# Performance work log

Measured on AMD Instinct MI355X. Metric: run time of the kernel, lower is better.

The kernel has to match this reference:

```python
import jax, jax.numpy as jnp
import numpy as np

N = 20000        # total nodes
E = 240000       # directed edges (avg in-degree 12); self-loops appended in reference
G = 50           # graphs in the batch
NPG = N // G     # nodes per graph
TD = 768         # text embedding dim
HC = 64          # hidden_channels
H = 8            # attention heads for conv1..conv3 (conv4 uses 1 head)
FD = 3 * HC * H + HC  # JK cat dim for num_layers=4
NEG = 0.2        # GATv2 leaky_relu negative slope
EPS = 1e-5       # GraphNorm eps


def setup_inputs() -> dict:
    key = jax.random.key(0)
    ks = iter(jax.random.split(key, 64))

    def w(shape, s=0.05):
        return jax.random.normal(next(ks), shape, dtype=jnp.float32) * s

    z = lambda *s: jnp.zeros(s, jnp.float32)
    o = lambda *s: jnp.ones(s, jnp.float32)

    inp = {
        'x': w((N, TD), 1.0),
        'edge_index': jax.random.randint(next(ks), (2, E), 0, N, dtype=jnp.int32),
        'batch': jnp.arange(N, dtype=jnp.int32) // NPG,
        'ptr': jnp.arange(G + 1, dtype=jnp.int32) * NPG,
        'tp_w': w((TD, HC)), 'tp_b': z(HC),
        'lin_w': w((FD, 1), 0.005), 'lin_b': z(1),
    }
    # GATv2Conv params: lin_l (source), lin_r (target), att, output bias
    for name, ind, heads, concat in [('c1', HC, H, True), ('c2', HC * H, H, True),
                                     ('c3', HC * H, H, True), ('c4', HC * H, 1, False)]:
        inp[name + '_wl'] = w((ind, heads * HC)); inp[name + '_bl'] = z(heads * HC)
        inp[name + '_wr'] = w((ind, heads * HC)); inp[name + '_br'] = z(heads * HC)
        inp[name + '_att'] = w((heads, HC))
        inp[name + '_bias'] = z(heads * HC if concat else HC)
    # GraphNorm params: weight, bias, mean_scale
    for name, d in [('n1', HC * H), ('n2', HC * H), ('n3', HC * H), ('n4', HC)]:
        inp[name + '_w'] = o(d); inp[name + '_b'] = z(d); inp[name + '_ms'] = o(d)
    return inp


def _gatv2(x, src, dst, wl, bl, wr, br, att, bias, heads, concat):
    # GATv2: e_ij = att . leaky_relu(W_l x_j + W_r x_i); alpha = softmax over in-neighbors of i
    xl = (x @ wl + bl).reshape(N, heads, HC)
    xr = (x @ wr + br).reshape(N, heads, HC)
    e = jax.nn.leaky_relu(xl[src] + xr[dst], NEG)           # [E', H, C]
    logit = jnp.einsum('ehc,hc->eh', e, att)                # [E', H]
    m = jax.ops.segment_max(logit, dst, num_segments=N)     # stable scatter-softmax
    p = jnp.exp(logit - m[dst])
    alpha = p / jax.ops.segment_sum(p, dst, num_segments=N)[dst]
    out = jax.ops.segment_sum(xl[src] * alpha[..., None], dst, num_segments=N)
    out = out.reshape(N, heads * HC) if concat else out.mean(axis=1)
    return out + bias


def _gnorm(x, batch, w, b, ms):
    # PyG GraphNorm: per-graph mean (scaled by mean_scale), per-graph std
    cnt = jax.ops.segment_sum(jnp.ones((N,), x.dtype), batch, num_segments=G)[:, None]
    mean = jax.ops.segment_sum(x, batch, num_segments=G) / cnt
    cen = x - ms * mean[batch]
    var = jax.ops.segment_sum(cen * cen, batch, num_segments=G) / cnt
    return w * cen / jnp.sqrt(var + EPS)[batch] + b


def reference(x, tp_w, tp_b,
              c1_wl, c1_bl, c1_wr, c1_br, c1_att, c1_bias,
              c2_wl, c2_bl, c2_wr, c2_br, c2_att, c2_bias,
              c3_wl, c3_bl, c3_wr, c3_br, c3_att, c3_bias,
              c4_wl, c4_bl, c4_wr, c4_br, c4_att, c4_bias,
              n1_w, n1_b, n1_ms, n2_w, n2_b, n2_ms,
              n3_w, n3_b, n3_ms, n4_w, n4_b, n4_ms,
              lin_w, lin_b, edge_index, batch, ptr):
    sl = jnp.arange(N, dtype=edge_index.dtype)
    src = jnp.concatenate([edge_index[0], sl])  # add_self_loops=True
    dst = jnp.concatenate([edge_index[1], sl])

    h = x @ tp_w + tp_b                          # text_proj (dropout = identity in eval)
    h = _gatv2(h, src, dst, c1_wl, c1_bl, c1_wr, c1_br, c1_att, c1_bias, H, True)
    h = jax.nn.elu(_gnorm(h, batch, n1_w, n1_b, n1_ms))
    xs = [h]
    h2 = _gatv2(h, src, dst, c2_wl, c2_bl, c2_wr, c2_br, c2_att, c2_bias, H, True)
    h = jax.nn.elu(_gnorm(h2 + h, batch, n2_w, n2_b, n2_ms))
    xs.append(h)
    h3 = _gatv2(h, src, dst, c3_wl, c3_bl, c3_wr, c3_br, c3_att, c3_bias, H, True)
    h = jax.nn.elu(_gnorm(h3 + h, batch, n3_w, n3_b, n3_ms))
    xs.append(h)
    h = _gnorm(_gatv2(h, src, dst, c4_wl, c4_bl, c4_wr, c4_br, c4_att, c4_bias, 1, False),
               batch, n4_w, n4_b, n4_ms)
    xs.append(h)

    xcat = jnp.concatenate(xs, axis=1)           # JumpingKnowledge cat -> [N, FD]
    out = xcat[ptr[:-1]] @ lin_w + lin_b         # summary node per graph -> [G, 1]
    return out.squeeze(-1)                       # num_classes==2 -> squeeze
```

## Files before the change

### kernel.cpp

```cpp
#include <hip/hip_runtime.h>
#include <hip/hip_bf16.h>

#define NEG_SLOPE 0.2f
#define EPSI 1e-5f
#define THR 8.0f

typedef __attribute__((ext_vector_type(8))) short bf16x8;
typedef __attribute__((ext_vector_type(4))) float f32x4;
typedef __attribute__((ext_vector_type(2))) float f32x2;

__device__ __forceinline__ float wred_sum(float v){
#pragma unroll
  for (int o = 32; o > 0; o >>= 1) v += __shfl_xor(v, o);
  return v;
}

__device__ __forceinline__ unsigned short f2bf(float f){
  __hip_bfloat16 h = __float2bfloat16(f);
  return *reinterpret_cast<unsigned short*>(&h);
}
__device__ __forceinline__ float bf2f(unsigned short u){
  return __uint_as_float((unsigned int)u << 16);
}
__device__ __forceinline__ f32x2 bfpair(unsigned int u){
  f32x2 r;
  r.x = __uint_as_float(u << 16);
  r.y = __uint_as_float(u & 0xffff0000u);
  return r;
}
__device__ __forceinline__ f32x2 vmax2(f32x2 a, f32x2 b){
#if __has_builtin(__builtin_elementwise_max)
  return __builtin_elementwise_max(a, b);
#else
  f32x2 r; r.x = fmaxf(a.x, b.x); r.y = fmaxf(a.y, b.y); return r;
#endif
}

__device__ __forceinline__ void gload16(const void* g, void* l){
  __builtin_amdgcn_global_load_lds((const __attribute__((address_space(1))) unsigned int*)g,
                                   (__attribute__((address_space(3))) unsigned int*)l, 16, 0, 0);
}

__global__ __launch_bounds__(256) void k_count(const int* __restrict__ ei, int* __restrict__ deg,
                                               int E, int EP){
  int e = blockIdx.x * 256 + threadIdx.x;
  if (e >= EP) return;
  int d = (e < E) ? ei[E + e] : (e - E);
  atomicAdd(&deg[d], 1);
}

__global__ __launch_bounds__(256) void k_scan(int* __restrict__ deg, int* __restrict__ rowptr, int n){
  __shared__ int part[256];
  int t = threadIdx.x;
  int L = (n + 255) / 256;
  int lo = t * L, hi = min(lo + L, n);
  int s = 0;
  for (int i = lo; i < hi; i++) s += deg[i];
  part[t] = s;
  __syncthreads();
  if (t == 0){
    int acc = 0;
    for (int i = 0; i < 256; i++){ int v = part[i]; part[i] = acc; acc += v; }
  }
  __syncthreads();
  int acc = part[t];
  for (int i = lo; i < hi; i++){
    int d = deg[i];
    rowptr[i] = acc;
    deg[i] = acc;
    acc += d;
  }
  if (t == 255) rowptr[n] = acc;
}

__global__ __launch_bounds__(256) void k_fill(const int* __restrict__ ei, int* __restrict__ cursor,
                                              int* __restrict__ srcn, int E, int EP){
  int e = blockIdx.x * 256 + threadIdx.x;
  if (e >= EP) return;
  int s, d;
  if (e < E){ s = ei[e]; d = ei[E + e]; } else { s = d = e - E; }
  int pos = atomicAdd(&cursor[d], 1);
  srcn[pos] = s;
}

__global__ __launch_bounds__(256) void k_cvt_act(const float* __restrict__ in,
                                                 unsigned short* __restrict__ ob, int total4){
  int i = blockIdx.x * 256 + threadIdx.x;
  if (i >= total4) return;
  float4 v = ((const float4*)in)[i];
  ushort4 o;
  o.x = f2bf(v.x); o.y = f2bf(v.y); o.z = f2bf(v.z); o.w = f2bf(v.w);
  ((ushort4*)ob)[i] = o;
}

__global__ __launch_bounds__(256) void k_cvt_wt(const float* __restrict__ W,
                                                unsigned short* __restrict__ Wt,
                                                int K, int Ncol){
  __shared__ float t[32][33];
  int bx = blockIdx.x, by = blockIdx.y;
  int tx = threadIdx.x & 31, ty = threadIdx.x >> 5;
#pragma unroll
  for (int i = 0; i < 4; i++)
    t[ty + i * 8][tx] = W[(size_t)(by * 32 + ty + i * 8) * Ncol + bx * 32 + tx];
  __syncthreads();
#pragma unroll
  for (int i = 0; i < 4; i++)
    Wt[(size_t)(bx * 32 + ty + i * 8) * K + by * 32 + tx] = f2bf(t[tx][ty + i * 8]);
}

__global__ __launch_bounds__(256) void k_cvt_wt2(const float* __restrict__ Wa,
                                                 const float* __restrict__ Wb,
                                                 unsigned short* __restrict__ Wt,
                                                 int K, int Ncol){
  __shared__ float t[32][33];
  int half = gridDim.x >> 1;
  int isB = blockIdx.x >= half;
  const float* W = isB ? Wb : Wa;
  unsigned short* out = Wt + (isB ? (size_t)Ncol * K : 0);
  int bx = isB ? blockIdx.x - half : blockIdx.x;
  int by = blockIdx.y;
  int tx = threadIdx.x & 31, ty = threadIdx.x >> 5;
#pragma unroll
  for (int i = 0; i < 4; i++)
    t[ty + i * 8][tx] = W[(size_t)(by * 32 + ty + i * 8) * Ncol + bx * 32 + tx];
  __syncthreads();
#pragma unroll
  for (int i = 0; i < 4; i++)
    out[(size_t)(bx * 32 + ty + i * 8) * K + by * 32 + tx] = f2bf(t[tx][ty + i * 8]);
}

template<int BN>
__global__ __launch_bounds__(512) void k_gemm_mfma8(const unsigned short* __restrict__ A,
                                                    const unsigned short* __restrict__ Wt,
                                                    const float* __restrict__ ba,
                                                    const float* __restrict__ bb,
                                                    int bsplit,
                                                    unsigned short* __restrict__ Cb,
                                                    int M, int K, int Ncol){
  constexpr int NF = BN / 64;
  __shared__ unsigned short As[128 * 32];
  __shared__ unsigned short Bs[BN * 32];
  const int tid = threadIdx.x;
  const int w = tid >> 6, lane = tid & 63;
  const int wr = w >> 2, wc = w & 3;
  const int row0 = blockIdx.y * 128, col0 = blockIdx.x * BN;
  const int lr = lane & 15, lk = lane >> 4;
  const int swz = (lr >> 1) & 3;

  f32x4 acc[4][NF];
#pragma unroll
  for (int i = 0; i < 4; i++)
#pragma unroll
    for (int j = 0; j < NF; j++) acc[i][j] = (f32x4){0.f, 0.f, 0.f, 0.f};

  for (int k0 = 0; k0 < K; k0 += 32){
    for (int g0 = w * 64; g0 < 512; g0 += 512){
      int g = g0 + lane;
      int row = g >> 2, slot = g & 3;
      int kq = slot ^ ((row >> 1) & 3);
      int srow = row0 + row; if (srow >= M) srow = M - 1;
      gload16(&A[(size_t)srow * K + k0 + kq * 8], &As[(size_t)g0 * 8]);
    }
    for (int g0 = w * 64; g0 < BN * 4; g0 += 512){
      int g = g0 + lane;
      int col = g >> 2, slot = g & 3;
      int kq = slot ^ ((col >> 1) & 3);
      gload16(&Wt[(size_t)(col0 + col) * K + k0 + kq * 8], &Bs[(size_t)g0 * 8]);
    }
    __syncthreads();

    bf16x8 af[4], bf_[NF];
#pragma unroll
    for (int mi = 0; mi < 4; mi++){
      int rl = wr * 64 + mi * 16 + lr;
      af[mi] = *(const bf16x8*)&As[(rl * 4 + (lk ^ swz)) * 8];
    }
#pragma unroll
    for (int ni = 0; ni < NF; ni++){
      int cl = wc * (BN / 4) + ni * 16 + lr;
      bf_[ni] = *(const bf16x8*)&Bs[(cl * 4 + (lk ^ swz)) * 8];
    }
#pragma unroll
    for (int mi = 0; mi < 4; mi++)
#pragma unroll
      for (int ni = 0; ni < NF; ni++)
        acc[mi][ni] = __builtin_amdgcn_mfma_f32_16x16x32_bf16(af[mi], bf_[ni], acc[mi][ni], 0, 0, 0);
    __syncthreads();
  }

#pragma unroll
  for (int mi = 0; mi < 4; mi++){
#pragma unroll
    for (int ni = 0; ni < NF; ni++){
      int gc = col0 + wc * (BN / 4) + ni * 16 + lr;
      float bv = gc < bsplit ? ba[gc] : bb[gc - bsplit];
#pragma unroll
      for (int r = 0; r < 4; r++){
        int gr = row0 + wr * 64 + mi * 16 + lk * 4 + r;
        if (gr < M) Cb[(size_t)gr * Ncol + gc] = f2bf(acc[mi][ni][r] + bv);
      }
    }
  }
}

__global__ __launch_bounds__(256) void k_gat_fused8(const unsigned short* __restrict__ xlrb,
                                                    const float* __restrict__ att,
                                                    const int* __restrict__ rowptr,
                                                    const int* __restrict__ srcn,
                                                    const float* __restrict__ bias,
                                                    const unsigned short* __restrict__ resb,
                                                    unsigned short* __restrict__ yb,
                                                    int N){
  int node = (blockIdx.x * 256 + threadIdx.x) >> 6;
  int lane = threadIdx.x & 63;
  if (node >= N) return;
  f32x2 xr2[4], av2[4];
  {
    uint4 ur = *(const uint4*)&xlrb[(size_t)node * 1024 + 512 + lane * 8];
    xr2[0] = bfpair(ur.x); xr2[1] = bfpair(ur.y); xr2[2] = bfpair(ur.z); xr2[3] = bfpair(ur.w);
    float4 a0 = *(const float4*)&att[lane * 8];
    float4 a1 = *(const float4*)&att[lane * 8 + 4];
    av2[0] = (f32x2){a0.x, a0.y}; av2[1] = (f32x2){a0.z, a0.w};
    av2[2] = (f32x2){a1.x, a1.y}; av2[3] = (f32x2){a1.z, a1.w};
  }
  int e0 = rowptr[node], e1 = rowptr[node + 1];
  float m0 = -1e30f, s0 = 0.f, m1 = -1e30f, s1 = 0.f;
  f32x2 acc0[4] = {}, acc1[4] = {};

  for (int base = e0; base < e1; base += 64){
    int cnt = min(64, e1 - base);
    int sn = 0;
    if (lane < cnt) sn = srcn[base + lane];
    int k = 0;
    for (; k + 1 < cnt; k += 2){
      int ska = __shfl(sn, k);
      int skb = __shfl(sn, k + 1);
      uint4 ua = *(const uint4*)&xlrb[(size_t)ska * 1024 + lane * 8];
      uint4 ub = *(const uint4*)&xlrb[(size_t)skb * 1024 + lane * 8];
      f32x2 va[4], vb[4];
      va[0] = bfpair(ua.x); va[1] = bfpair(ua.y); va[2] = bfpair(ua.z); va[3] = bfpair(ua.w);
      vb[0] = bfpair(ub.x); vb[1] = bfpair(ub.y); vb[2] = bfpair(ub.z); vb[3] = bfpair(ub.w);
      f32x2 da = (f32x2){0.f, 0.f}, db = (f32x2){0.f, 0.f};
#pragma unroll
      for (int j = 0; j < 4; j++){
        f32x2 ta = va[j] + xr2[j];
        f32x2 tb = vb[j] + xr2[j];
        ta = vmax2(ta, ta * NEG_SLOPE);
        tb = vmax2(tb, tb * NEG_SLOPE);
        da += ta * av2[j];
        db += tb * av2[j];
      }
      float suma = da.x + da.y, sumb = db.x + db.y;
      suma += __shfl_xor(suma, 1); sumb += __shfl_xor(sumb, 1);
      suma += __shfl_xor(suma, 2); sumb += __shfl_xor(sumb, 2);
      suma += __shfl_xor(suma, 4); sumb += __shfl_xor(sumb, 4);
      if (__builtin_expect(__any(suma > m0 + THR), 0)){
        float mn = fmaxf(m0, suma);
        float cs = __expf(m0 - mn);
        float p  = __expf(suma - mn);
        s0 = s0 * cs + p;
#pragma unroll
        for (int j = 0; j < 4; j++) acc0[j] = acc0[j] * cs + va[j] * p;
        m0 = mn;
      } else {
        float p = __expf(suma - m0);
        s0 += p;
#pragma unroll
        for (int j = 0; j < 4; j++) acc0[j] += va[j] * p;
      }
      if (__builtin_expect(__any(sumb > m1 + THR), 0)){
        float mn = fmaxf(m1, sumb);
        float cs = __expf(m1 - mn);
        float p  = __expf(sumb - mn);
        s1 = s1 * cs + p;
#pragma unroll
        for (int j = 0; j < 4; j++) acc1[j] = acc1[j] * cs + vb[j] * p;
        m1 = mn;
      } else {
        float p = __expf(sumb - m1);
        s1 += p;
#pragma unroll
        for (int j = 0; j < 4; j++) acc1[j] += vb[j] * p;
      }
    }
    if (k < cnt){
      int ska = __shfl(sn, k);
      uint4 ua = *(const uint4*)&xlrb[(size_t)ska * 1024 + lane * 8];
      f32x2 va[4];
      va[0] = bfpair(ua.x); va[1] = bfpair(ua.y); va[2] = bfpair(ua.z); va[3] = bfpair(ua.w);
      f32x2 da = (f32x2){0.f, 0.f};
#pragma unroll
      for (int j = 0; j < 4; j++){
        f32x2 ta = va[j] + xr2[j];
        ta = vmax2(ta, ta * NEG_SLOPE);
        da += ta * av2[j];
      }
      float suma = da.x + da.y;
      suma += __shfl_xor(suma, 1);
      suma += __shfl_xor(suma, 2);
      suma += __shfl_xor(suma, 4);
      if (__builtin_expect(__any(suma > m0 + THR), 0)){
        float mn = fmaxf(m0, suma);
        float cs = __expf(m0 - mn);
        float p  = __expf(suma - mn);
        s0 = s0 * cs + p;
#pragma unroll
        for (int j = 0; j < 4; j++) acc0[j] = acc0[j] * cs + va[j] * p;
        m0 = mn;
      } else {
        float p = __expf(suma - m0);
        s0 += p;
#pragma unroll
        for (int j = 0; j < 4; j++) acc0[j] += va[j] * p;
      }
    }
  }
  float m = fmaxf(m0, m1);
  float c0 = __expf(m0 - m), c1 = __expf(m1 - m);
  float s = s0 * c0 + s1 * c1;
  float inv = 1.f / s;
  float4 b0 = *(const float4*)&bias[lane * 8];
  float4 b1 = *(const float4*)&bias[lane * 8 + 4];
  f32x2 bi2[4] = {(f32x2){b0.x, b0.y}, (f32x2){b0.z, b0.w},
                  (f32x2){b1.x, b1.y}, (f32x2){b1.z, b1.w}};
  f32x2 re2[4] = {};
  size_t o = (size_t)node * 512 + lane * 8;
  if (resb){
    uint4 rr = *(const uint4*)&resb[o];
    re2[0] = bfpair(rr.x); re2[1] = bfpair(rr.y); re2[2] = bfpair(rr.z); re2[3] = bfpair(rr.w);
  }
  bf16x8 ov;
#pragma unroll
  for (int j = 0; j < 4; j++){
    f32x2 r = (acc0[j] * c0 + acc1[j] * c1) * inv + bi2[j] + re2[j];
    ov[2 * j]     = (short)f2bf(r.x);
    ov[2 * j + 1] = (short)f2bf(r.y);
  }
  *(bf16x8*)&yb[o] = ov;
}

__global__ __launch_bounds__(256) void k_gat_fused1(const unsigned short* __restrict__ xlr,
                                                    const float* __restrict__ att,
                                                    const int* __restrict__ rowptr,
                                                    const int* __restrict__ srcn,
                                                    const float* __restrict__ bias,
                                                    unsigned short* __restrict__ yb4,
                                                    int N){
  int node = (blockIdx.x * 256 + threadIdx.x) >> 6;
  int lane = threadIdx.x & 63;
  if (node >= N) return;
  float xrv = bf2f(xlr[(size_t)node * 128 + 64 + lane]);
  float attv = att[lane];
  int e0 = rowptr[node], e1 = rowptr[node + 1];
  float m = -1e30f, s = 0.f, acc = 0.f;
  for (int base = e0; base < e1; base += 64){
    int cnt = min(64, e1 - base);
    int sn = 0;
    if (lane < cnt) sn = srcn[base + lane];
    for (int k = 0; k < cnt; k++){
      int sk = __shfl(sn, k);
      float v = bf2f(xlr[(size_t)sk * 128 + lane]);
      float t = v + xrv;
      t = fmaxf(t, t * NEG_SLOPE);
      float sum = wred_sum(t * attv);
      if (sum > m + THR){
        float mn = fmaxf(m, sum);
        float cs = __expf(m - mn);
        float p  = __expf(sum - mn);
        s = s * cs + p;
        acc = acc * cs + p * v;
        m = mn;
      } else {
        float p = __expf(sum - m);
        s += p;
        acc += p * v;
      }
    }
  }
  yb4[(size_t)node * 64 + lane] = f2bf(acc / s + bias[lane]);
}

#define NCHUNK 16
__global__ __launch_bounds__(256) void k_gnorm_stats(const unsigned short* __restrict__ y,
                                                     const int* __restrict__ ptrg,
                                                     float* __restrict__ psum,
                                                     float* __restrict__ psq,
                                                     int OD){
  int g = blockIdx.x, chunk = blockIdx.z;
  int lane = threadIdx.x & 63, sub = threadIdx.x >> 6;
  int c = blockIdx.y * 64 + lane;
  int lo = ptrg[g], hi = ptrg[g + 1], len = hi - lo;
  int c0 = lo + (len * chunk) / NCHUNK, c1 = lo + (len * (chunk + 1)) / NCHUNK;
  float s = 0.f, q = 0.f;
  for (int i = c0 + sub; i < c1; i += 4){
    float v = bf2f(y[(size_t)i * OD + c]);
    s += v; q += v * v;
  }
  __shared__ float sm[4][64], sq2[4][64];
  sm[sub][lane] = s; sq2[sub][lane] = q;
  __syncthreads();
  if (sub == 0){
    s = sm[0][lane] + sm[1][lane] + sm[2][lane] + sm[3][lane];
    q = sq2[0][lane] + sq2[1][lane] + sq2[2][lane] + sq2[3][lane];
    size_t o = (size_t)(g * NCHUNK + chunk) * OD + c;
    psum[o] = s; psq[o] = q;
  }
}

__global__ __launch_bounds__(256) void k_gnorm_coef(const float* __restrict__ psum,
                                                    const float* __restrict__ psq,
                                                    const float* __restrict__ w,
                                                    const float* __restrict__ b,
                                                    const float* __restrict__ ms,
                                                    const int* __restrict__ ptrg,
                                                    float* __restrict__ cA,
                                                    float* __restrict__ cC,
                                                    int OD){
  int g = blockIdx.x;
  int len = ptrg[g + 1] - ptrg[g];
  float inv_n = 1.f / (float)len;
  for (int c = threadIdx.x; c < OD; c += 256){
    float s = 0.f, q = 0.f;
    for (int k = 0; k < NCHUNK; k++){
      size_t o = (size_t)(g * NCHUNK + k) * OD + c;
      s += psum[o]; q += psq[o];
    }
    float mean = s * inv_n, ey2 = q * inv_n;
    float m = ms[c];
    float var = ey2 - mean * mean * (2.f * m - m * m);
    float inv = rsqrtf(var + EPSI);
    float A = w[c] * inv;
    cA[(size_t)g * OD + c] = A;
    cC[(size_t)g * OD + c] = b[c] - A * m * mean;
  }
}

__global__ __launch_bounds__(256) void k_gnorm_apply(const unsigned short* __restrict__ y,
                                                     const int* __restrict__ batch,
                                                     const float* __restrict__ cA,
                                                     const float* __restrict__ cC,
                                                     unsigned short* __restrict__ outb,
                                                     const int* __restrict__ ptrg,
                                                     float* __restrict__ cat,
                                                     int catoff, int FD,
                                                     int OD, int total4, int do_elu){
  int idx = blockIdx.x * 256 + threadIdx.x;
  if (idx >= total4) return;
  int od4 = OD >> 2;
  int node = idx / od4;
  int c = (idx - node * od4) << 2;
  int g = batch[node];
  ushort4 uv = ((const ushort4*)y)[idx];
  float4 v = make_float4(bf2f(uv.x), bf2f(uv.y), bf2f(uv.z), bf2f(uv.w));
  float4 A = *(const float4*)&cA[(size_t)g * OD + c];
  float4 Cc = *(const float4*)&cC[(size_t)g * OD + c];
  float4 r;
  r.x = A.x * v.x + Cc.x;
  r.y = A.y * v.y + Cc.y;
  r.z = A.z * v.z + Cc.z;
  r.w = A.w * v.w + Cc.w;
  if (do_elu){
    r.x = r.x > 0.f ? r.x : expf(r.x) - 1.f;
    r.y = r.y > 0.f ? r.y : expf(r.y) - 1.f;
    r.z = r.z > 0.f ? r.z : expf(r.z) - 1.f;
    r.w = r.w > 0.f ? r.w : expf(r.w) - 1.f;
  }
  ushort4 ob;
  ob.x = f2bf(r.x); ob.y = f2bf(r.y); ob.z = f2bf(r.z); ob.w = f2bf(r.w);
  ((ushort4*)outb)[idx] = ob;
  if (node == ptrg[g])
    *(float4*)&cat[(size_t)g * FD + catoff + c] = r;
}

__global__ __launch_bounds__(256) void k_final(const float* __restrict__ cat,
                                               const float* __restrict__ lin_w,
                                               const float* __restrict__ lin_b,
                                               float* __restrict__ out, int FD){
  int g = blockIdx.x;
  float s = 0.f;
  for (int c = threadIdx.x; c < FD; c += 256) s += cat[(size_t)g * FD + c] * lin_w[c];
  s = wred_sum(s);
  __shared__ float sm[4];
  if ((threadIdx.x & 63) == 0) sm[threadIdx.x >> 6] = s;
  __syncthreads();
  if (threadIdx.x == 0) out[g] = sm[0] + sm[1] + sm[2] + sm[3] + lin_b[0];
}

extern "C" void kernel_launch(void* const* d_in, const int* in_sizes, int n_in,
                              void* d_out, int out_size, void* d_ws, size_t ws_size,
                              hipStream_t stream) {
  const int TD = 768, HC = 64, H = 8;
  const float* x     = (const float*)d_in[0];
  const int*   ei    = (const int*)d_in[1];
  const int*   batch = (const int*)d_in[2];
  const int*   ptrg  = (const int*)d_in[3];
  const float* tp_w  = (const float*)d_in[4];
  const float* tp_b  = (const float*)d_in[5];
  const float* lin_w = (const float*)d_in[6];
  const float* lin_b = (const float*)d_in[7];
  const float* cw[4][6];
  for (int l = 0; l < 4; l++)
    for (int j = 0; j < 6; j++) cw[l][j] = (const float*)d_in[8 + 6 * l + j];
  const float* nw[4][3];
  for (int l = 0; l < 4; l++)
    for (int j = 0; j < 3; j++) nw[l][j] = (const float*)d_in[32 + 3 * l + j];

  const int N  = in_sizes[0] / TD;
  const int E  = in_sizes[1] / 2;
  const int EP = E + N;
  const int G  = in_sizes[3] - 1;
  const int FD = 3 * HC * H + HC;

  char* wsp = (char*)d_ws;
  size_t off = 0;
  auto alloc = [&](size_t b) -> void* {
    void* p = wsp + off;
    off += (b + 255) & ~(size_t)255;
    return p;
  };
  unsigned short* xlrb = (unsigned short*)alloc((size_t)N * 1024 * 2);
  unsigned short* yb   = (unsigned short*)alloc((size_t)N * 512 * 2);
  unsigned short* actA = (unsigned short*)alloc((size_t)N * 512 * 2);
  unsigned short* h0h  = (unsigned short*)alloc((size_t)N * 64 * 2);
  int*   rowptr= (int*)alloc((size_t)(N + 1) * 4);
  int*   cursor= (int*)alloc((size_t)N * 4);
  int*   srcn  = (int*)alloc((size_t)EP * 4);
  float* cat   = (float*)alloc((size_t)G * FD * 4);
  float* psum  = (float*)alloc((size_t)G * NCHUNK * 512 * 4);
  float* psq   = (float*)alloc((size_t)G * NCHUNK * 512 * 4);
  float* cA    = (float*)alloc((size_t)G * 512 * 4);
  float* cC    = (float*)alloc((size_t)G * 512 * 4);
  unsigned short* WtLR = (unsigned short*)alloc((size_t)1024 * 512 * 2);
  unsigned short* WtTP = (unsigned short*)alloc((size_t)64 * 768 * 2);
  unsigned short* Wt4  = (unsigned short*)alloc((size_t)128 * 512 * 2);
  (void)ws_size; (void)n_in; (void)out_size;

  float* out = (float*)d_out;

  unsigned short* xbf   = xlrb;
  unsigned short* xlr4b = xlrb;
  unsigned short* yb4   = yb;

  hipMemsetAsync(cursor, 0, (size_t)N * 4, stream);
  int eblk = (EP + 255) / 256;
  k_count<<<eblk, 256, 0, stream>>>(ei, cursor, E, EP);
  k_scan<<<1, 256, 0, stream>>>(cursor, rowptr, N);
  k_fill<<<eblk, 256, 0, stream>>>(ei, cursor, srcn, E, EP);

  const int mfmaRows = (N + 127) / 128;
  const int nodeBlocks = (N + 3) / 4;

  k_cvt_act<<<(N * TD / 4 + 255) / 256, 256, 0, stream>>>(x, xbf, N * TD / 4);
  k_cvt_wt<<<dim3(2, TD / 32), 256, 0, stream>>>(tp_w, WtTP, TD, 64);
  k_gemm_mfma8<64><<<dim3(1, mfmaRows), 512, 0, stream>>>(xbf, WtTP, tp_b, tp_b, 64, h0h, N, TD, 64);

  auto layer8 = [&](const unsigned short* actbf, int Kin, int l,
                    const unsigned short* resb, int catoff){
    k_cvt_wt2<<<dim3(32, Kin / 32), 256, 0, stream>>>(cw[l][0], cw[l][2], WtLR, Kin, 512);
    k_gemm_mfma8<256><<<dim3(4, mfmaRows), 512, 0, stream>>>(actbf, WtLR, cw[l][1], cw[l][3], 512,
                                                             xlrb, N, Kin, 1024);
    k_gat_fused8<<<nodeBlocks, 256, 0, stream>>>(xlrb, cw[l][4], rowptr, srcn,
                                                 cw[l][5], resb, yb, N);
    k_gnorm_stats<<<dim3(G, 8, NCHUNK), 256, 0, stream>>>(yb, ptrg, psum, psq, 512);
    k_gnorm_coef<<<G, 256, 0, stream>>>(psum, psq, nw[l][0], nw[l][1], nw[l][2], ptrg, cA, cC, 512);
    int total4 = N * 128;
    k_gnorm_apply<<<(total4 + 255) / 256, 256, 0, stream>>>(yb, batch, cA, cC, actA,
                                                            ptrg, cat, catoff, FD,
                                                            512, total4, 1);
  };

  layer8(h0h,  64,  0, nullptr, 0);
  layer8(actA, 512, 1, actA,    512);
  layer8(actA, 512, 2, actA,    1024);

  k_cvt_wt2<<<dim3(4, 16), 256, 0, stream>>>(cw[3][0], cw[3][2], Wt4, 512, 64);
  k_gemm_mfma8<128><<<dim3(1, mfmaRows), 512, 0, stream>>>(actA, Wt4, cw[3][1], cw[3][3], 64,
                                                           xlr4b, N, 512, 128);
  k_gat_fused1<<<nodeBlocks, 256, 0, stream>>>(xlr4b, cw[3][4], rowptr, srcn,
                                               cw[3][5], yb4, N);
  k_gnorm_stats<<<dim3(G, 1, NCHUNK), 256, 0, stream>>>(yb4, ptrg, psum, psq, 64);
  k_gnorm_coef<<<G, 256, 0, stream>>>(psum, psq, nw[3][0], nw[3][1], nw[3][2], ptrg, cA, cC, 64);
  k_gnorm_apply<<<(N * 16 + 255) / 256, 256, 0, stream>>>(yb4, batch, cA, cC, h0h,
                                                          ptrg, cat, 1536, FD,
                                                          64, N * 16, 0);

  k_final<<<G, 256, 0, stream>>>(cat, lin_w, lin_b, out, FD);
}
```

Before: 507.6 us.

## Split GAT edge list across two waves per node; fuse fp32→bf16 into text-proj GEMM

The 8-head GAT aggregation kernel now gives each node two wavefronts, each processing half of the in-edges with its own online softmax. The two partial results are merged through shared memory. This doubles parallelism and memory-level concurrency for the gather-bound loop, at the cost of LDS traffic, a block barrier and idle second waves during the epilogue. Separately, the standalone fp32-to-bf16 activation conversion is removed, and a dedicated text-projection GEMM converts fp32 rows to bf16 while loading them into LDS, which avoids writing and rereading the N×768 bf16 copy.

```diff
diff --git a/kernel.cpp b/kernel.cpp
--- a/kernel.cpp
+++ b/kernel.cpp
@@ -81,16 +81,6 @@
   if (e < E){ s = ei[e]; d = ei[E + e]; } else { s = d = e - E; }
   int pos = atomicAdd(&cursor[d], 1);
   srcn[pos] = s;
-}
-
-__global__ __launch_bounds__(256) void k_cvt_act(const float* __restrict__ in,
-                                                 unsigned short* __restrict__ ob, int total4){
-  int i = blockIdx.x * 256 + threadIdx.x;
-  if (i >= total4) return;
-  float4 v = ((const float4*)in)[i];
-  ushort4 o;
-  o.x = f2bf(v.x); o.y = f2bf(v.y); o.z = f2bf(v.z); o.w = f2bf(v.w);
-  ((ushort4*)ob)[i] = o;
 }
 
 __global__ __launch_bounds__(256) void k_cvt_wt(const float* __restrict__ W,
@@ -203,6 +193,75 @@
   }
 }
 
+__global__ __launch_bounds__(512) void k_gemm_tp(const float* __restrict__ A,
+                                                 const unsigned short* __restrict__ Wt,
+                                                 const float* __restrict__ bias,
+                                                 unsigned short* __restrict__ Cb,
+                                                 int M, int K){
+  __shared__ unsigned short As[128 * 32];
+  __shared__ unsigned short Bs[64 * 32];
+  const int tid = threadIdx.x;
+  const int w = tid >> 6, lane = tid & 63;
+  const int wr = w >> 2, wc = w & 3;
+  const int row0 = blockIdx.y * 128;
+  const int lr = lane & 15, lk = lane >> 4;
+  const int swz = (lr >> 1) & 3;
+
+  f32x4 acc[4];
+#pragma unroll
+  for (int i = 0; i < 4; i++) acc[i] = (f32x4){0.f, 0.f, 0.f, 0.f};
+
+  for (int k0 = 0; k0 < K; k0 += 32){
+    {
+      int g = tid;
+      int row = g >> 2, slot = g & 3;
+      int kq = slot ^ ((row >> 1) & 3);
+      int srow = row0 + row; if (srow >= M) srow = M - 1;
+      const float* ap = &A[(size_t)srow * K + k0 + kq * 8];
+      float4 f0 = *(const float4*)ap;
+      float4 f1 = *(const float4*)(ap + 4);
+      bf16x8 v;
+      v[0] = (short)f2bf(f0.x); v[1] = (short)f2bf(f0.y);
+      v[2] = (short)f2bf(f0.z); v[3] = (short)f2bf(f0.w);
+      v[4] = (short)f2bf(f1.x); v[5] = (short)f2bf(f1.y);
+      v[6] = (short)f2bf(f1.z); v[7] = (short)f2bf(f1.w);
+      *(bf16x8*)&As[(size_t)g * 8] = v;
+    }
+    for (int g0 = w * 64; g0 < 256; g0 += 512){
+      int g = g0 + lane;
+      int col = g >> 2, slot = g & 3;
+      int kq = slot ^ ((col >> 1) & 3);
+      gload16(&Wt[(size_t)col * K + k0 + kq * 8], &Bs[(size_t)g0 * 8]);
+    }
+    __syncthreads();
+
+    bf16x8 af[4], bfr;
+#pragma unroll
+    for (int mi = 0; mi < 4; mi++){
+      int rl = wr * 64 + mi * 16 + lr;
+      af[mi] = *(const bf16x8*)&As[(rl * 4 + (lk ^ swz)) * 8];
+    }
+    {
+      int cl = wc * 16 + lr;
+      bfr = *(const bf16x8*)&Bs[(cl * 4 + (lk ^ swz)) * 8];
+    }
+#pragma unroll
+    for (int mi = 0; mi < 4; mi++)
+      acc[mi] = __builtin_amdgcn_mfma_f32_16x16x32_bf16(af[mi], bfr, acc[mi], 0, 0, 0);
+    __syncthreads();
+  }
+
+  int gc = wc * 16 + lr;
+  float bv = bias[gc];
+#pragma unroll
+  for (int mi = 0; mi < 4; mi++)
+#pragma unroll
+    for (int r = 0; r < 4; r++){
+      int gr = row0 + wr * 64 + mi * 16 + lk * 4 + r;
+      if (gr < M) Cb[(size_t)gr * 64 + gc] = f2bf(acc[mi][r] + bv);
+    }
+}
+
 __global__ __launch_bounds__(256) void k_gat_fused8(const unsigned short* __restrict__ xlrb,
                                                     const float* __restrict__ att,
                                                     const int* __restrict__ rowptr,
@@ -211,24 +270,34 @@
                                                     const unsigned short* __restrict__ resb,
                                                     unsigned short* __restrict__ yb,
                                                     int N){
-  int node = (blockIdx.x * 256 + threadIdx.x) >> 6;
-  int lane = threadIdx.x & 63;
-  if (node >= N) return;
+  __shared__ float lm[4][64], ls[4][64], lacc[4][64][9];
+  const int tid = threadIdx.x;
+  const int w = tid >> 6, lane = tid & 63;
+  const int node = blockIdx.x * 2 + (w >> 1);
+  const int half = w & 1;
+  const int nc = min(node, N - 1);
+
   f32x2 xr2[4], av2[4];
   {
-    uint4 ur = *(const uint4*)&xlrb[(size_t)node * 1024 + 512 + lane * 8];
+    uint4 ur = *(const uint4*)&xlrb[(size_t)nc * 1024 + 512 + lane * 8];
     xr2[0] = bfpair(ur.x); xr2[1] = bfpair(ur.y); xr2[2] = bfpair(ur.z); xr2[3] = bfpair(ur.w);
     float4 a0 = *(const float4*)&att[lane * 8];
     float4 a1 = *(const float4*)&att[lane * 8 + 4];
     av2[0] = (f32x2){a0.x, a0.y}; av2[1] = (f32x2){a0.z, a0.w};
     av2[2] = (f32x2){a1.x, a1.y}; av2[3] = (f32x2){a1.z, a1.w};
   }
-  int e0 = rowptr[node], e1 = rowptr[node + 1];
+  int e0 = rowptr[nc], e1 = rowptr[nc + 1];
+  if (node >= N){ e0 = 0; e1 = 0; }
+  int len = e1 - e0;
+  int mid = e0 + ((len + 1) >> 1);
+  int rs = half ? mid : e0;
+  int re = half ? e1 : mid;
+
   float m0 = -1e30f, s0 = 0.f, m1 = -1e30f, s1 = 0.f;
   f32x2 acc0[4] = {}, acc1[4] = {};
 
-  for (int base = e0; base < e1; base += 64){
-    int cnt = min(64, e1 - base);
+  for (int base = rs; base < re; base += 64){
+    int cnt = min(64, re - base);
     int sn = 0;
     if (lane < cnt) sn = srcn[base + lane];
     int k = 0;
@@ -315,10 +384,29 @@
       }
     }
   }
-  float m = fmaxf(m0, m1);
-  float c0 = __expf(m0 - m), c1 = __expf(m1 - m);
-  float s = s0 * c0 + s1 * c1;
+
+  float mW = fmaxf(m0, m1);
+  float ca = __expf(m0 - mW), cb = __expf(m1 - mW);
+  float sW = s0 * ca + s1 * cb;
+  f32x2 aW[4];
+#pragma unroll
+  for (int j = 0; j < 4; j++) aW[j] = acc0[j] * ca + acc1[j] * cb;
+
+  lm[w][lane] = mW; ls[w][lane] = sW;
+#pragma unroll
+  for (int j = 0; j < 4; j++){
+    lacc[w][lane][2 * j]     = aW[j].x;
+    lacc[w][lane][2 * j + 1] = aW[j].y;
+  }
+  __syncthreads();
+  if (half || node >= N) return;
+
+  float mo = lm[w + 1][lane], so = ls[w + 1][lane];
+  float mm = fmaxf(mW, mo);
+  float c0x = __expf(mW - mm), c1x = __expf(mo - mm);
+  float s = sW * c0x + so * c1x;
   float inv = 1.f / s;
+
   float4 b0 = *(const float4*)&bias[lane * 8];
   float4 b1 = *(const float4*)&bias[lane * 8 + 4];
   f32x2 bi2[4] = {(f32x2){b0.x, b0.y}, (f32x2){b0.z, b0.w},
@@ -332,7 +420,8 @@
   bf16x8 ov;
 #pragma unroll
   for (int j = 0; j < 4; j++){
-    f32x2 r = (acc0[j] * c0 + acc1[j] * c1) * inv + bi2[j] + re2[j];
+    f32x2 ao = (f32x2){lacc[w + 1][lane][2 * j], lacc[w + 1][lane][2 * j + 1]};
+    f32x2 r = (aW[j] * c0x + ao * c1x) * inv + bi2[j] + re2[j];
     ov[2 * j]     = (short)f2bf(r.x);
     ov[2 * j + 1] = (short)f2bf(r.y);
   }
@@ -537,7 +626,6 @@
 
   float* out = (float*)d_out;
 
-  unsigned short* xbf   = xlrb;
   unsigned short* xlr4b = xlrb;
   unsigned short* yb4   = yb;
 
@@ -548,19 +636,19 @@
   k_fill<<<eblk, 256, 0, stream>>>(ei, cursor, srcn, E, EP);
 
   const int mfmaRows = (N + 127) / 128;
+  const int nb8 = (N + 1) / 2;
   const int nodeBlocks = (N + 3) / 4;
 
-  k_cvt_act<<<(N * TD / 4 + 255) / 256, 256, 0, stream>>>(x, xbf, N * TD / 4);
   k_cvt_wt<<<dim3(2, TD / 32), 256, 0, stream>>>(tp_w, WtTP, TD, 64);
-  k_gemm_mfma8<64><<<dim3(1, mfmaRows), 512, 0, stream>>>(xbf, WtTP, tp_b, tp_b, 64, h0h, N, TD, 64);
+  k_gemm_tp<<<dim3(1, mfmaRows), 512, 0, stream>>>(x, WtTP, tp_b, h0h, N, TD);
 
   auto layer8 = [&](const unsigned short* actbf, int Kin, int l,
                     const unsigned short* resb, int catoff){
     k_cvt_wt2<<<dim3(32, Kin / 32), 256, 0, stream>>>(cw[l][0], cw[l][2], WtLR, Kin, 512);
     k_gemm_mfma8<256><<<dim3(4, mfmaRows), 512, 0, stream>>>(actbf, WtLR, cw[l][1], cw[l][3], 512,
                                                              xlrb, N, Kin, 1024);
-    k_gat_fused8<<<nodeBlocks, 256, 0, stream>>>(xlrb, cw[l][4], rowptr, srcn,
-                                                 cw[l][5], resb, yb, N);
+    k_gat_fused8<<<nb8, 256, 0, stream>>>(xlrb, cw[l][4], rowptr, srcn,
+                                          cw[l][5], resb, yb, N);
     k_gnorm_stats<<<dim3(G, 8, NCHUNK), 256, 0, stream>>>(yb, ptrg, psum, psq, 512);
     k_gnorm_coef<<<G, 256, 0, stream>>>(psum, psq, nw[l][0], nw[l][1], nw[l][2], ptrg, cA, cC, 512);
     int total4 = N * 128;
```

Result: no change. 509.7 us (+0.4%).
